# Kernel optimization log

Measured on AMD Instinct MI355X. Metric: run time of the kernel, lower is better.

## Reference

```python
import jax, jax.numpy as jnp
import numpy as np

E = 8            # moe_num_experts
FFN = 8192       # ffn_hidden_size
D = 2048         # d_model
B, T = 1, 4096


def setup_inputs() -> dict:
    key = jax.random.key(0)
    k1, k2, k3, k4 = jax.random.split(key, 4)
    x = jax.random.normal(k1, (B, T, D), dtype=jnp.float32)
    # params stored flat as (E*FFN, D), as in the flax module
    w1 = jax.random.normal(k2, (E * FFN, D), dtype=jnp.float32) * 0.02
    v1 = jax.random.normal(k3, (E * FFN, D), dtype=jnp.float32) * 0.02
    w2 = jax.random.normal(k4, (E * FFN, D), dtype=jnp.float32) * 0.02
    return {"x": x, "w1": w1, "v1": v1, "w2": w2, "expert_idx": 3}


def reference(x, w1, v1, w2, expert_idx):
    # select this expert's weight slabs: (FFN, D) each
    expert_shape = (E, FFN, D)
    ew1 = w1.reshape(expert_shape)[expert_idx]
    ev1 = v1.reshape(expert_shape)[expert_idx]
    ew2 = w2.reshape(expert_shape)[expert_idx]
    # gate and up projections: [B,T,D] x [D,FFN] -> [B,T,FFN]
    x1 = jnp.einsum('btd,fd->btf', x, ew1)
    x2 = jnp.einsum('btd,fd->btf', x, ev1)
    h = jax.nn.silu(x1) * x2
    # down projection (note: matmul with ew2, i.e. contraction over FFN)
    out = jnp.einsum('btf,fd->btd', h, ew2)
    return out
```

## Files before the change

kernel.cpp:

```cpp
#include <hip/hip_runtime.h>

#define E_NUM 8
#define FFN_DIM 8192
#define D_DIM 2048
#define T_DIM 4096

using bf16x8 = __attribute__((ext_vector_type(8))) short;
using f32x4  = __attribute__((ext_vector_type(4))) float;
using u16x8  = __attribute__((ext_vector_type(8))) unsigned short;

__device__ __forceinline__ unsigned short f2bf(float f) {
  union { float f; unsigned int u; } v; v.f = f;
  unsigned int u = v.u;
  unsigned int r = (u + 0x7FFFu + ((u >> 16) & 1u)) >> 16;
  return (unsigned short)r;
}

__device__ __forceinline__ void gload16(const unsigned short* g, const unsigned short* l) {
  __builtin_amdgcn_global_load_lds(
      (const __attribute__((address_space(1))) void*)g,
      (__attribute__((address_space(3))) void*)l, 16, 0, 0);
}

__global__ void convert_kernel(const float* __restrict__ src_base,
                               const int* __restrict__ eidx, long slab,
                               unsigned short* __restrict__ dst, long n) {
  const float* src = src_base + (long)(*eidx) * slab;
  long stride = (long)gridDim.x * blockDim.x;
  for (long i = (long)blockIdx.x * blockDim.x + threadIdx.x; i * 8 < n; i += stride) {
    long e = i * 8;
    const float4* p = (const float4*)(src + e);
    float4 f0 = p[0], f1 = p[1];
    u16x8 o;
    o[0] = f2bf(f0.x); o[1] = f2bf(f0.y); o[2] = f2bf(f0.z); o[3] = f2bf(f0.w);
    o[4] = f2bf(f1.x); o[5] = f2bf(f1.y); o[6] = f2bf(f1.z); o[7] = f2bf(f1.w);
    *(u16x8*)(dst + e) = o;
  }
}

__global__ void transpose_kernel(const float* __restrict__ w2,
                                 const int* __restrict__ eidx,
                                 unsigned short* __restrict__ dst) {
  __shared__ unsigned short tile[32][33];
  const float* src = w2 + (long)(*eidx) * (long)FFN_DIM * D_DIM;
  int d0 = blockIdx.x << 5;
  int f0 = blockIdx.y << 5;
  int tx = threadIdx.x & 31, ty = threadIdx.x >> 5;
#pragma unroll
  for (int i = 0; i < 4; ++i) {
    int f = ty + i * 8;
    tile[f][tx] = f2bf(src[(long)(f0 + f) * D_DIM + d0 + tx]);
  }
  __syncthreads();
#pragma unroll
  for (int i = 0; i < 4; ++i) {
    int d = ty + i * 8;
    dst[(long)(d0 + d) * FFN_DIM + f0 + tx] = tile[tx][d];
  }
}

#define VMCNT8 asm volatile("s_waitcnt vmcnt(8)" ::: "memory")
#define VMCNT6 asm volatile("s_waitcnt vmcnt(6)" ::: "memory")
#define VMCNT2 asm volatile("s_waitcnt vmcnt(2)" ::: "memory")
#define VMCNT0 asm volatile("s_waitcnt vmcnt(0)" ::: "memory")
#define BAR __builtin_amdgcn_s_barrier()

__global__ __launch_bounds__(512, 2) void gemm1_silu(
    const unsigned short* __restrict__ Xb,
    const unsigned short* __restrict__ W1b,
    const unsigned short* __restrict__ V1b,
    unsigned short* __restrict__ Hb) {
  __shared__ __align__(16) unsigned short sA[2 * 256 * 64];
  __shared__ __align__(16) unsigned short sB1[2 * 128 * 64];
  __shared__ __align__(16) unsigned short sB2[2 * 128 * 64];

  const int tid = threadIdx.x;
  const int wv = tid >> 6, l = tid & 63;
  const int wm = wv >> 1, wn = wv & 1;
  const int kq = l >> 4, lr = l & 15;
  const int m0 = blockIdx.y << 8;
  const int n0 = blockIdx.x << 7;

  const int rsub = tid >> 3;
  const int sslot8 = ((tid & 7) ^ ((tid >> 3) & 7)) << 3;
  const unsigned short* gA0  = Xb  + (long)(m0 + rsub) * D_DIM + sslot8;
  const unsigned short* gB1r = W1b + (long)(n0 + rsub) * D_DIM + sslot8;
  const unsigned short* gB2r = V1b + (long)(n0 + rsub) * D_DIM + sslot8;

#define ST_A(r_)  gload16(gA0  + (long)((r_) * 64) * D_DIM + tc, sA  + sb * 16384 + (r_) * 4096 + wv * 512)
#define ST_B1(r_) gload16(gB1r + (long)((r_) * 64) * D_DIM + tc, sB1 + sb * 8192  + (r_) * 4096 + wv * 512)
#define ST_B2(r_) gload16(gB2r + (long)((r_) * 64) * D_DIM + tc, sB2 + sb * 8192  + (r_) * 4096 + wv * 512)

  int raoff[4], rboff[4];
#pragma unroll
  for (int m = 0; m < 4; ++m) {
    int row = wm * 64 + m * 16 + lr;
    raoff[m] = row * 64 + ((kq ^ (row & 7)) << 3);
  }
#pragma unroll
  for (int n = 0; n < 4; ++n) {
    int row = wn * 64 + n * 16 + lr;
    rboff[n] = row * 64 + ((kq ^ (row & 7)) << 3);
  }

  f32x4 acc1[4][4], acc2[4][4];
  f32x4 z = {0.f, 0.f, 0.f, 0.f};
#pragma unroll
  for (int m = 0; m < 4; ++m)
#pragma unroll
    for (int n = 0; n < 4; ++n) { acc1[m][n] = z; acc2[m][n] = z; }

  {
    int tc = 0, sb = 0;
    ST_A(0); ST_A(1); ST_A(2); ST_A(3);
    ST_B1(0); ST_B1(1); ST_B2(0); ST_B2(1);
    VMCNT2;
    BAR;
  }

  const int NT = D_DIM / 64;
  for (int t = 0; t < NT; ++t) {
    const int db = t & 1;
    const unsigned short* Ab  = sA  + db * 16384;
    const unsigned short* B1b = sB1 + db * 8192;
    const unsigned short* B2b = sB2 + db * 8192;
    const int pf = (t < NT - 1);
    const int tc = (t + 1) << 6;
    const int sb = db ^ 1;
    bf16x8 af[4], bf_[4];

#pragma unroll
    for (int m = 0; m < 4; ++m) af[m] = *(const bf16x8*)(Ab + raoff[m]);
#pragma unroll
    for (int n = 0; n < 4; ++n) bf_[n] = *(const bf16x8*)(B1b + rboff[n]);
    if (pf) {
      ST_A(0); ST_A(1); ST_A(2); ST_A(3);
      ST_B1(0); ST_B1(1); ST_B2(0); ST_B2(1);
    }
    BAR;
    __builtin_amdgcn_s_setprio(1);
#pragma unroll
    for (int m = 0; m < 4; ++m)
#pragma unroll
      for (int n = 0; n < 4; ++n)
        acc1[m][n] = __builtin_amdgcn_mfma_f32_16x16x32_bf16(af[m], bf_[n], acc1[m][n], 0, 0, 0);
    __builtin_amdgcn_s_setprio(0);
    if (pf) { VMCNT8; } else { VMCNT0; }
    BAR;

#pragma unroll
    for (int n = 0; n < 4; ++n) bf_[n] = *(const bf16x8*)(B2b + rboff[n]);
    BAR;
    __builtin_amdgcn_s_setprio(1);
#pragma unroll
    for (int m = 0; m < 4; ++m)
#pragma unroll
      for (int n = 0; n < 4; ++n)
        acc2[m][n] = __builtin_amdgcn_mfma_f32_16x16x32_bf16(af[m], bf_[n], acc2[m][n], 0, 0, 0);
    __builtin_amdgcn_s_setprio(0);
    BAR;

#pragma unroll
    for (int m = 0; m < 4; ++m) af[m] = *(const bf16x8*)(Ab + (raoff[m] ^ 32));
#pragma unroll
    for (int n = 0; n < 4; ++n) bf_[n] = *(const bf16x8*)(B1b + (rboff[n] ^ 32));
    BAR;
    __builtin_amdgcn_s_setprio(1);
#pragma unroll
    for (int m = 0; m < 4; ++m)
#pragma unroll
      for (int n = 0; n < 4; ++n)
        acc1[m][n] = __builtin_amdgcn_mfma_f32_16x16x32_bf16(af[m], bf_[n], acc1[m][n], 0, 0, 0);
    __builtin_amdgcn_s_setprio(0);
    BAR;

#pragma unroll
    for (int n = 0; n < 4; ++n) bf_[n] = *(const bf16x8*)(B2b + (rboff[n] ^ 32));
    BAR;
    __builtin_amdgcn_s_setprio(1);
#pragma unroll
    for (int m = 0; m < 4; ++m)
#pragma unroll
      for (int n = 0; n < 4; ++n)
        acc2[m][n] = __builtin_amdgcn_mfma_f32_16x16x32_bf16(af[m], bf_[n], acc2[m][n], 0, 0, 0);
    __builtin_amdgcn_s_setprio(0);
    if (pf) { VMCNT2; }
    BAR;
  }

#pragma unroll
  for (int m = 0; m < 4; ++m)
#pragma unroll
    for (int n = 0; n < 4; ++n)
#pragma unroll
      for (int r = 0; r < 4; ++r) {
        int row = m0 + wm * 64 + m * 16 + kq * 4 + r;
        int col = n0 + wn * 64 + n * 16 + lr;
        float x1 = acc1[m][n][r], x2 = acc2[m][n][r];
        float hv = x1 / (1.f + __expf(-x1)) * x2;
        Hb[(long)row * FFN_DIM + col] = f2bf(hv);
      }
#undef ST_A
#undef ST_B1
#undef ST_B2
}

__global__ __launch_bounds__(512, 2) void gemm2(
    const unsigned short* __restrict__ Hb,
    const unsigned short* __restrict__ W2T,
    float* __restrict__ out) {
  __shared__ __align__(16) unsigned short sA[3 * 256 * 64];
  __shared__ __align__(16) unsigned short sB[3 * 128 * 64];

  const int tid = threadIdx.x;
  const int wv = tid >> 6, l = tid & 63;
  const int wm = wv >> 1, wn = wv & 1;
  const int kq = l >> 4, lr = l & 15;
  const int m0 = blockIdx.y << 8;
  const int n0 = blockIdx.x << 7;

  const int rsub = tid >> 3;
  const int sslot8 = ((tid & 7) ^ ((tid >> 3) & 7)) << 3;
  const unsigned short* gA0  = Hb  + (long)(m0 + rsub) * FFN_DIM + sslot8;
  const unsigned short* gB0r = W2T + (long)(n0 + rsub) * FFN_DIM + sslot8;

#define ST2_A(r_) gload16(gA0  + (long)((r_) * 64) * FFN_DIM + tc2, sA + bwr * 16384 + (r_) * 4096 + wv * 512)
#define ST2_B(r_) gload16(gB0r + (long)((r_) * 64) * FFN_DIM + tc2, sB + bwr * 8192  + (r_) * 4096 + wv * 512)

  int raoff[4], rboff[4];
#pragma unroll
  for (int m = 0; m < 4; ++m) {
    int row = wm * 64 + m * 16 + lr;
    raoff[m] = row * 64 + ((kq ^ (row & 7)) << 3);
  }
#pragma unroll
  for (int n = 0; n < 4; ++n) {
    int row = wn * 64 + n * 16 + lr;
    rboff[n] = row * 64 + ((kq ^ (row & 7)) << 3);
  }

  f32x4 acc[4][4];
  f32x4 z = {0.f, 0.f, 0.f, 0.f};
#pragma unroll
  for (int m = 0; m < 4; ++m)
#pragma unroll
    for (int n = 0; n < 4; ++n) acc[m][n] = z;

  {
    int tc2 = 0, bwr = 0;
    ST2_A(0); ST2_A(1); ST2_A(2); ST2_A(3); ST2_B(0); ST2_B(1);
    tc2 = 64; bwr = 1;
    ST2_A(0); ST2_A(1); ST2_A(2); ST2_A(3); ST2_B(0); ST2_B(1);
    VMCNT6;
    BAR;
  }

  const int NT = FFN_DIM / 64;
  int brd = 0;
  for (int t = 0; t < NT; ++t) {
    const unsigned short* Ab = sA + brd * 16384;
    const unsigned short* Bb = sB + brd * 8192;
    const int pf2 = (t + 2 < NT);
    const int tc2 = (t + 2) << 6;
    const int bwr = (brd + 2 >= 3) ? brd - 1 : brd + 2;
    bf16x8 af[4], bf_[4];

#pragma unroll
    for (int m = 0; m < 4; ++m) af[m] = *(const bf16x8*)(Ab + raoff[m]);
#pragma unroll
    for (int n = 0; n < 4; ++n) bf_[n] = *(const bf16x8*)(Bb + rboff[n]);
    if (pf2) {
      ST2_A(0); ST2_A(1); ST2_A(2); ST2_A(3); ST2_B(0); ST2_B(1);
    }
    BAR;
    __builtin_amdgcn_s_setprio(1);
#pragma unroll
    for (int m = 0; m < 4; ++m)
#pragma unroll
      for (int n = 0; n < 4; ++n)
        acc[m][n] = __builtin_amdgcn_mfma_f32_16x16x32_bf16(af[m], bf_[n], acc[m][n], 0, 0, 0);
    __builtin_amdgcn_s_setprio(0);
    BAR;

#pragma unroll
    for (int m = 0; m < 4; ++m) af[m] = *(const bf16x8*)(Ab + (raoff[m] ^ 32));
#pragma unroll
    for (int n = 0; n < 4; ++n) bf_[n] = *(const bf16x8*)(Bb + (rboff[n] ^ 32));
    BAR;
    __builtin_amdgcn_s_setprio(1);
#pragma unroll
    for (int m = 0; m < 4; ++m)
#pragma unroll
      for (int n = 0; n < 4; ++n)
        acc[m][n] = __builtin_amdgcn_mfma_f32_16x16x32_bf16(af[m], bf_[n], acc[m][n], 0, 0, 0);
    __builtin_amdgcn_s_setprio(0);
    if (pf2) { VMCNT6; } else if (t + 1 < NT) { VMCNT0; }
    BAR;

    brd = (brd + 1 == 3) ? 0 : brd + 1;
  }

#pragma unroll
  for (int m = 0; m < 4; ++m)
#pragma unroll
    for (int n = 0; n < 4; ++n)
#pragma unroll
      for (int r = 0; r < 4; ++r) {
        int row = m0 + wm * 64 + m * 16 + kq * 4 + r;
        int col = n0 + wn * 64 + n * 16 + lr;
        out[(long)row * D_DIM + col] = acc[m][n][r];
      }
#undef ST2_A
#undef ST2_B
}

extern "C" void kernel_launch(void* const* d_in, const int* in_sizes, int n_in,
                              void* d_out, int out_size, void* d_ws, size_t ws_size,
                              hipStream_t stream) {
  const float* x  = (const float*)d_in[0];
  const float* w1 = (const float*)d_in[1];
  const float* v1 = (const float*)d_in[2];
  const float* w2 = (const float*)d_in[3];
  const int* eidx = (const int*)d_in[4];

  char* ws = (char*)d_ws;
  unsigned short* Xb  = (unsigned short*)(ws);
  unsigned short* W1b = (unsigned short*)(ws + (16l << 20));
  unsigned short* V1b = (unsigned short*)(ws + (48l << 20));
  unsigned short* W2T = (unsigned short*)(ws + (80l << 20));
  unsigned short* Hb  = (unsigned short*)(ws + (112l << 20));
  float* out = (float*)d_out;

  long slab = (long)FFN_DIM * D_DIM;
  convert_kernel<<<2048, 256, 0, stream>>>(x,  eidx, 0,    Xb,  (long)T_DIM * D_DIM);
  convert_kernel<<<2048, 256, 0, stream>>>(w1, eidx, slab, W1b, slab);
  convert_kernel<<<2048, 256, 0, stream>>>(v1, eidx, slab, V1b, slab);
  transpose_kernel<<<dim3(D_DIM / 32, FFN_DIM / 32), 256, 0, stream>>>(w2, eidx, W2T);
  gemm1_silu<<<dim3(FFN_DIM / 128, T_DIM / 256), 512, 0, stream>>>(Xb, W1b, V1b, Hb);
  gemm2<<<dim3(D_DIM / 128, T_DIM / 256), 512, 0, stream>>>(Hb, W2T, out);
}
```

Baseline: 538.4 us.

## Restructure both GEMMs into 8-wave ping-pong schedules with staggered per-quadrant prefetch

Both GEMM kernels get a new main loop. It works in four quadrant phases, and each phase issues a slice of the next tiles' global-to-LDS loads, so memory traffic is spread across the iteration instead of bunched in one burst. gemm1 changes its wave layout to 2x4 with each wave covering two 128-row halves, and gemm2 drops from triple to double buffering while splitting A into halves. The goal is better overlap of loads with MFMA work and less LDS use. The trade-offs are more barriers per iteration and tighter vmcnt accounting, where a miscount could expose load latency or give wrong results.

```diff
diff --git a/kernel.cpp b/kernel.cpp
--- a/kernel.cpp
+++ b/kernel.cpp
@@ -59,20 +59,175 @@
   }
 }
 
-#define VMCNT8 asm volatile("s_waitcnt vmcnt(8)" ::: "memory")
 #define VMCNT6 asm volatile("s_waitcnt vmcnt(6)" ::: "memory")
-#define VMCNT2 asm volatile("s_waitcnt vmcnt(2)" ::: "memory")
+#define VMCNT4 asm volatile("s_waitcnt vmcnt(4)" ::: "memory")
 #define VMCNT0 asm volatile("s_waitcnt vmcnt(0)" ::: "memory")
 #define BAR __builtin_amdgcn_s_barrier()
+#define PRIO1 __builtin_amdgcn_s_setprio(1)
+#define PRIO0 __builtin_amdgcn_s_setprio(0)
 
 __global__ __launch_bounds__(512, 2) void gemm1_silu(
     const unsigned short* __restrict__ Xb,
     const unsigned short* __restrict__ W1b,
     const unsigned short* __restrict__ V1b,
     unsigned short* __restrict__ Hb) {
-  __shared__ __align__(16) unsigned short sA[2 * 256 * 64];
-  __shared__ __align__(16) unsigned short sB1[2 * 128 * 64];
-  __shared__ __align__(16) unsigned short sB2[2 * 128 * 64];
+  __shared__ __align__(16) unsigned short sA[2 * 2 * 8192];
+  __shared__ __align__(16) unsigned short sB1[2 * 8192];
+  __shared__ __align__(16) unsigned short sB2[2 * 8192];
+
+  const int tid = threadIdx.x;
+  const int wv = tid >> 6, l = tid & 63;
+  const int wm = wv >> 2, wn = wv & 3;
+  const int kq = l >> 4, lr = l & 15;
+  const int m0 = blockIdx.y << 8;
+  const int n0 = blockIdx.x << 7;
+
+  const int rsub = tid >> 3;
+  const int sslot8 = ((tid & 7) ^ ((tid >> 3) & 7)) << 3;
+  const unsigned short* gA  = Xb  + (long)(m0 + rsub) * D_DIM + sslot8;
+  const unsigned short* gB1 = W1b + (long)(n0 + rsub) * D_DIM + sslot8;
+  const unsigned short* gB2 = V1b + (long)(n0 + rsub) * D_DIM + sslot8;
+
+#define STG(gbase, rowoff, tc_, lbase) do { \
+    gload16((gbase) + (long)(rowoff) * D_DIM + (tc_), (lbase) + wv * 512); \
+    gload16((gbase) + (long)((rowoff) + 64) * D_DIM + (tc_), (lbase) + 4096 + wv * 512); \
+  } while (0)
+
+  int aoff[4], boff[2];
+#pragma unroll
+  for (int j = 0; j < 4; ++j) {
+    int row = wm * 64 + j * 16 + lr;
+    aoff[j] = row * 64 + ((kq ^ (row & 7)) << 3);
+  }
+#pragma unroll
+  for (int g = 0; g < 2; ++g) {
+    int row = wn * 32 + g * 16 + lr;
+    boff[g] = row * 64 + ((kq ^ (row & 7)) << 3);
+  }
+
+  f32x4 acc1[8][2], acc2[8][2];
+  f32x4 z = {0.f, 0.f, 0.f, 0.f};
+#pragma unroll
+  for (int f = 0; f < 8; ++f)
+#pragma unroll
+    for (int g = 0; g < 2; ++g) { acc1[f][g] = z; acc2[f][g] = z; }
+
+  STG(gA, 0, 0, sA);
+  STG(gA, 128, 0, sA + 8192);
+  STG(gB1, 0, 0, sB1);
+  STG(gB2, 0, 0, sB2);
+  STG(gA, 0, 64, sA + 16384);
+  STG(gA, 128, 64, sA + 24576);
+  STG(gB1, 0, 64, sB1 + 8192);
+  VMCNT6;
+  BAR;
+
+  const int NT = D_DIM / 64;
+  for (int t = 0; t < NT; ++t) {
+    const int db = t & 1, sx = db ^ 1;
+    const unsigned short* A0p = sA + (db * 2 + 0) * 8192;
+    const unsigned short* A1p = sA + (db * 2 + 1) * 8192;
+    const unsigned short* B1p = sB1 + db * 8192;
+    const unsigned short* B2p = sB2 + db * 8192;
+    const int p1ok = (t + 1 < NT), p2ok = (t + 2 < NT);
+    const int tc1 = (t + 1) << 6, tc2 = (t + 2) << 6;
+    bf16x8 aA[4][2], aB[4][2], b1[2][2], b2[2][2];
+
+#pragma unroll
+    for (int j = 0; j < 4; ++j) {
+      aA[j][0] = *(const bf16x8*)(A0p + aoff[j]);
+      aA[j][1] = *(const bf16x8*)(A0p + (aoff[j] ^ 32));
+    }
+#pragma unroll
+    for (int g = 0; g < 2; ++g) {
+      b1[g][0] = *(const bf16x8*)(B1p + boff[g]);
+      b1[g][1] = *(const bf16x8*)(B1p + (boff[g] ^ 32));
+    }
+    if (p1ok) STG(gB2, 0, tc1, sB2 + sx * 8192);
+    BAR;
+    PRIO1;
+#pragma unroll
+    for (int j = 0; j < 4; ++j)
+#pragma unroll
+      for (int g = 0; g < 2; ++g) {
+        acc1[j][g] = __builtin_amdgcn_mfma_f32_16x16x32_bf16(aA[j][0], b1[g][0], acc1[j][g], 0, 0, 0);
+        acc1[j][g] = __builtin_amdgcn_mfma_f32_16x16x32_bf16(aA[j][1], b1[g][1], acc1[j][g], 0, 0, 0);
+      }
+    PRIO0;
+    BAR;
+
+#pragma unroll
+    for (int j = 0; j < 4; ++j) {
+      aB[j][0] = *(const bf16x8*)(A1p + aoff[j]);
+      aB[j][1] = *(const bf16x8*)(A1p + (aoff[j] ^ 32));
+    }
+    if (p2ok) STG(gA, 0, tc2, sA + (db * 2 + 0) * 8192);
+    BAR;
+    PRIO1;
+#pragma unroll
+    for (int j = 0; j < 4; ++j)
+#pragma unroll
+      for (int g = 0; g < 2; ++g) {
+        acc1[4 + j][g] = __builtin_amdgcn_mfma_f32_16x16x32_bf16(aB[j][0], b1[g][0], acc1[4 + j][g], 0, 0, 0);
+        acc1[4 + j][g] = __builtin_amdgcn_mfma_f32_16x16x32_bf16(aB[j][1], b1[g][1], acc1[4 + j][g], 0, 0, 0);
+      }
+    PRIO0;
+    BAR;
+
+#pragma unroll
+    for (int g = 0; g < 2; ++g) {
+      b2[g][0] = *(const bf16x8*)(B2p + boff[g]);
+      b2[g][1] = *(const bf16x8*)(B2p + (boff[g] ^ 32));
+    }
+    if (p2ok) STG(gA, 128, tc2, sA + (db * 2 + 1) * 8192);
+    BAR;
+    PRIO1;
+#pragma unroll
+    for (int j = 0; j < 4; ++j)
+#pragma unroll
+      for (int g = 0; g < 2; ++g) {
+        acc2[j][g] = __builtin_amdgcn_mfma_f32_16x16x32_bf16(aA[j][0], b2[g][0], acc2[j][g], 0, 0, 0);
+        acc2[j][g] = __builtin_amdgcn_mfma_f32_16x16x32_bf16(aA[j][1], b2[g][1], acc2[j][g], 0, 0, 0);
+      }
+    PRIO0;
+    BAR;
+
+    if (p2ok) STG(gB1, 0, tc2, sB1 + db * 8192);
+    BAR;
+    PRIO1;
+#pragma unroll
+    for (int j = 0; j < 4; ++j)
+#pragma unroll
+      for (int g = 0; g < 2; ++g) {
+        acc2[4 + j][g] = __builtin_amdgcn_mfma_f32_16x16x32_bf16(aB[j][0], b2[g][0], acc2[4 + j][g], 0, 0, 0);
+        acc2[4 + j][g] = __builtin_amdgcn_mfma_f32_16x16x32_bf16(aB[j][1], b2[g][1], acc2[4 + j][g], 0, 0, 0);
+      }
+    PRIO0;
+    if (p2ok) { VMCNT6; } else if (p1ok) { VMCNT0; }
+    BAR;
+  }
+
+#pragma unroll
+  for (int f = 0; f < 8; ++f)
+#pragma unroll
+    for (int g = 0; g < 2; ++g)
+#pragma unroll
+      for (int r = 0; r < 4; ++r) {
+        int row = m0 + (f >> 2) * 128 + wm * 64 + (f & 3) * 16 + kq * 4 + r;
+        int col = n0 + wn * 32 + g * 16 + lr;
+        float x1 = acc1[f][g][r], x2 = acc2[f][g][r];
+        float hv = x1 / (1.f + __expf(-x1)) * x2;
+        Hb[(long)row * FFN_DIM + col] = f2bf(hv);
+      }
+#undef STG
+}
+
+__global__ __launch_bounds__(512, 2) void gemm2(
+    const unsigned short* __restrict__ Hb,
+    const unsigned short* __restrict__ W2T,
+    float* __restrict__ out) {
+  __shared__ __align__(16) unsigned short sA[2 * 2 * 8192];
+  __shared__ __align__(16) unsigned short sB[2 * 8192];
 
   const int tid = threadIdx.x;
   const int wv = tid >> 6, l = tid & 63;
@@ -80,238 +235,138 @@
   const int kq = l >> 4, lr = l & 15;
   const int m0 = blockIdx.y << 8;
   const int n0 = blockIdx.x << 7;
+  const int hA = wm >> 1;
 
   const int rsub = tid >> 3;
   const int sslot8 = ((tid & 7) ^ ((tid >> 3) & 7)) << 3;
-  const unsigned short* gA0  = Xb  + (long)(m0 + rsub) * D_DIM + sslot8;
-  const unsigned short* gB1r = W1b + (long)(n0 + rsub) * D_DIM + sslot8;
-  const unsigned short* gB2r = V1b + (long)(n0 + rsub) * D_DIM + sslot8;
-
-#define ST_A(r_)  gload16(gA0  + (long)((r_) * 64) * D_DIM + tc, sA  + sb * 16384 + (r_) * 4096 + wv * 512)
-#define ST_B1(r_) gload16(gB1r + (long)((r_) * 64) * D_DIM + tc, sB1 + sb * 8192  + (r_) * 4096 + wv * 512)
-#define ST_B2(r_) gload16(gB2r + (long)((r_) * 64) * D_DIM + tc, sB2 + sb * 8192  + (r_) * 4096 + wv * 512)
-
-  int raoff[4], rboff[4];
-#pragma unroll
-  for (int m = 0; m < 4; ++m) {
-    int row = wm * 64 + m * 16 + lr;
-    raoff[m] = row * 64 + ((kq ^ (row & 7)) << 3);
-  }
-#pragma unroll
-  for (int n = 0; n < 4; ++n) {
-    int row = wn * 64 + n * 16 + lr;
-    rboff[n] = row * 64 + ((kq ^ (row & 7)) << 3);
-  }
-
-  f32x4 acc1[4][4], acc2[4][4];
-  f32x4 z = {0.f, 0.f, 0.f, 0.f};
-#pragma unroll
-  for (int m = 0; m < 4; ++m)
-#pragma unroll
-    for (int n = 0; n < 4; ++n) { acc1[m][n] = z; acc2[m][n] = z; }
-
-  {
-    int tc = 0, sb = 0;
-    ST_A(0); ST_A(1); ST_A(2); ST_A(3);
-    ST_B1(0); ST_B1(1); ST_B2(0); ST_B2(1);
-    VMCNT2;
-    BAR;
-  }
-
-  const int NT = D_DIM / 64;
-  for (int t = 0; t < NT; ++t) {
-    const int db = t & 1;
-    const unsigned short* Ab  = sA  + db * 16384;
-    const unsigned short* B1b = sB1 + db * 8192;
-    const unsigned short* B2b = sB2 + db * 8192;
-    const int pf = (t < NT - 1);
-    const int tc = (t + 1) << 6;
-    const int sb = db ^ 1;
-    bf16x8 af[4], bf_[4];
-
-#pragma unroll
-    for (int m = 0; m < 4; ++m) af[m] = *(const bf16x8*)(Ab + raoff[m]);
-#pragma unroll
-    for (int n = 0; n < 4; ++n) bf_[n] = *(const bf16x8*)(B1b + rboff[n]);
-    if (pf) {
-      ST_A(0); ST_A(1); ST_A(2); ST_A(3);
-      ST_B1(0); ST_B1(1); ST_B2(0); ST_B2(1);
-    }
-    BAR;
-    __builtin_amdgcn_s_setprio(1);
-#pragma unroll
-    for (int m = 0; m < 4; ++m)
-#pragma unroll
-      for (int n = 0; n < 4; ++n)
-        acc1[m][n] = __builtin_amdgcn_mfma_f32_16x16x32_bf16(af[m], bf_[n], acc1[m][n], 0, 0, 0);
-    __builtin_amdgcn_s_setprio(0);
-    if (pf) { VMCNT8; } else { VMCNT0; }
-    BAR;
-
-#pragma unroll
-    for (int n = 0; n < 4; ++n) bf_[n] = *(const bf16x8*)(B2b + rboff[n]);
-    BAR;
-    __builtin_amdgcn_s_setprio(1);
-#pragma unroll
-    for (int m = 0; m < 4; ++m)
-#pragma unroll
-      for (int n = 0; n < 4; ++n)
-        acc2[m][n] = __builtin_amdgcn_mfma_f32_16x16x32_bf16(af[m], bf_[n], acc2[m][n], 0, 0, 0);
-    __builtin_amdgcn_s_setprio(0);
-    BAR;
-
-#pragma unroll
-    for (int m = 0; m < 4; ++m) af[m] = *(const bf16x8*)(Ab + (raoff[m] ^ 32));
-#pragma unroll
-    for (int n = 0; n < 4; ++n) bf_[n] = *(const bf16x8*)(B1b + (rboff[n] ^ 32));
-    BAR;
-    __builtin_amdgcn_s_setprio(1);
-#pragma unroll
-    for (int m = 0; m < 4; ++m)
-#pragma unroll
-      for (int n = 0; n < 4; ++n)
-        acc1[m][n] = __builtin_amdgcn_mfma_f32_16x16x32_bf16(af[m], bf_[n], acc1[m][n], 0, 0, 0);
-    __builtin_amdgcn_s_setprio(0);
-    BAR;
-
-#pragma unroll
-    for (int n = 0; n < 4; ++n) bf_[n] = *(const bf16x8*)(B2b + (rboff[n] ^ 32));
-    BAR;
-    __builtin_amdgcn_s_setprio(1);
-#pragma unroll
-    for (int m = 0; m < 4; ++m)
-#pragma unroll
-      for (int n = 0; n < 4; ++n)
-        acc2[m][n] = __builtin_amdgcn_mfma_f32_16x16x32_bf16(af[m], bf_[n], acc2[m][n], 0, 0, 0);
-    __builtin_amdgcn_s_setprio(0);
-    if (pf) { VMCNT2; }
-    BAR;
-  }
-
-#pragma unroll
-  for (int m = 0; m < 4; ++m)
-#pragma unroll
-    for (int n = 0; n < 4; ++n)
-#pragma unroll
-      for (int r = 0; r < 4; ++r) {
-        int row = m0 + wm * 64 + m * 16 + kq * 4 + r;
-        int col = n0 + wn * 64 + n * 16 + lr;
-        float x1 = acc1[m][n][r], x2 = acc2[m][n][r];
-        float hv = x1 / (1.f + __expf(-x1)) * x2;
-        Hb[(long)row * FFN_DIM + col] = f2bf(hv);
-      }
-#undef ST_A
-#undef ST_B1
-#undef ST_B2
-}
-
-__global__ __launch_bounds__(512, 2) void gemm2(
-    const unsigned short* __restrict__ Hb,
-    const unsigned short* __restrict__ W2T,
-    float* __restrict__ out) {
-  __shared__ __align__(16) unsigned short sA[3 * 256 * 64];
-  __shared__ __align__(16) unsigned short sB[3 * 128 * 64];
-
-  const int tid = threadIdx.x;
-  const int wv = tid >> 6, l = tid & 63;
-  const int wm = wv >> 1, wn = wv & 1;
-  const int kq = l >> 4, lr = l & 15;
-  const int m0 = blockIdx.y << 8;
-  const int n0 = blockIdx.x << 7;
-
-  const int rsub = tid >> 3;
-  const int sslot8 = ((tid & 7) ^ ((tid >> 3) & 7)) << 3;
-  const unsigned short* gA0  = Hb  + (long)(m0 + rsub) * FFN_DIM + sslot8;
-  const unsigned short* gB0r = W2T + (long)(n0 + rsub) * FFN_DIM + sslot8;
-
-#define ST2_A(r_) gload16(gA0  + (long)((r_) * 64) * FFN_DIM + tc2, sA + bwr * 16384 + (r_) * 4096 + wv * 512)
-#define ST2_B(r_) gload16(gB0r + (long)((r_) * 64) * FFN_DIM + tc2, sB + bwr * 8192  + (r_) * 4096 + wv * 512)
-
-  int raoff[4], rboff[4];
-#pragma unroll
-  for (int m = 0; m < 4; ++m) {
-    int row = wm * 64 + m * 16 + lr;
-    raoff[m] = row * 64 + ((kq ^ (row & 7)) << 3);
-  }
-#pragma unroll
-  for (int n = 0; n < 4; ++n) {
-    int row = wn * 64 + n * 16 + lr;
-    rboff[n] = row * 64 + ((kq ^ (row & 7)) << 3);
+  const unsigned short* gA = Hb  + (long)(m0 + rsub) * FFN_DIM + sslot8;
+  const unsigned short* gB = W2T + (long)(n0 + rsub) * FFN_DIM + sslot8;
+
+#define STG2(gbase, rowoff, tc_, lbase) do { \
+    gload16((gbase) + (long)(rowoff) * FFN_DIM + (tc_), (lbase) + wv * 512); \
+    gload16((gbase) + (long)((rowoff) + 64) * FFN_DIM + (tc_), (lbase) + 4096 + wv * 512); \
+  } while (0)
+
+  int aoff[4], boff[4];
+#pragma unroll
+  for (int f = 0; f < 4; ++f) {
+    int row = (wm & 1) * 64 + f * 16 + lr;
+    aoff[f] = row * 64 + ((kq ^ (row & 7)) << 3);
+  }
+#pragma unroll
+  for (int g = 0; g < 4; ++g) {
+    int row = wn * 64 + g * 16 + lr;
+    boff[g] = row * 64 + ((kq ^ (row & 7)) << 3);
   }
 
   f32x4 acc[4][4];
   f32x4 z = {0.f, 0.f, 0.f, 0.f};
 #pragma unroll
-  for (int m = 0; m < 4; ++m)
-#pragma unroll
-    for (int n = 0; n < 4; ++n) acc[m][n] = z;
-
-  {
-    int tc2 = 0, bwr = 0;
-    ST2_A(0); ST2_A(1); ST2_A(2); ST2_A(3); ST2_B(0); ST2_B(1);
-    tc2 = 64; bwr = 1;
-    ST2_A(0); ST2_A(1); ST2_A(2); ST2_A(3); ST2_B(0); ST2_B(1);
-    VMCNT6;
-    BAR;
-  }
+  for (int f = 0; f < 4; ++f)
+#pragma unroll
+    for (int g = 0; g < 4; ++g) acc[f][g] = z;
+
+  STG2(gA, 0, 0, sA);
+  STG2(gA, 128, 0, sA + 8192);
+  STG2(gB, 0, 0, sB);
+  STG2(gA, 0, 64, sA + 16384);
+  STG2(gA, 128, 64, sA + 24576);
+  VMCNT4;
+  BAR;
 
   const int NT = FFN_DIM / 64;
-  int brd = 0;
   for (int t = 0; t < NT; ++t) {
-    const unsigned short* Ab = sA + brd * 16384;
-    const unsigned short* Bb = sB + brd * 8192;
-    const int pf2 = (t + 2 < NT);
-    const int tc2 = (t + 2) << 6;
-    const int bwr = (brd + 2 >= 3) ? brd - 1 : brd + 2;
-    bf16x8 af[4], bf_[4];
-
-#pragma unroll
-    for (int m = 0; m < 4; ++m) af[m] = *(const bf16x8*)(Ab + raoff[m]);
-#pragma unroll
-    for (int n = 0; n < 4; ++n) bf_[n] = *(const bf16x8*)(Bb + rboff[n]);
-    if (pf2) {
-      ST2_A(0); ST2_A(1); ST2_A(2); ST2_A(3); ST2_B(0); ST2_B(1);
-    }
-    BAR;
-    __builtin_amdgcn_s_setprio(1);
-#pragma unroll
-    for (int m = 0; m < 4; ++m)
-#pragma unroll
-      for (int n = 0; n < 4; ++n)
-        acc[m][n] = __builtin_amdgcn_mfma_f32_16x16x32_bf16(af[m], bf_[n], acc[m][n], 0, 0, 0);
-    __builtin_amdgcn_s_setprio(0);
-    BAR;
-
-#pragma unroll
-    for (int m = 0; m < 4; ++m) af[m] = *(const bf16x8*)(Ab + (raoff[m] ^ 32));
-#pragma unroll
-    for (int n = 0; n < 4; ++n) bf_[n] = *(const bf16x8*)(Bb + (rboff[n] ^ 32));
-    BAR;
-    __builtin_amdgcn_s_setprio(1);
-#pragma unroll
-    for (int m = 0; m < 4; ++m)
-#pragma unroll
-      for (int n = 0; n < 4; ++n)
-        acc[m][n] = __builtin_amdgcn_mfma_f32_16x16x32_bf16(af[m], bf_[n], acc[m][n], 0, 0, 0);
-    __builtin_amdgcn_s_setprio(0);
-    if (pf2) { VMCNT6; } else if (t + 1 < NT) { VMCNT0; }
-    BAR;
-
-    brd = (brd + 1 == 3) ? 0 : brd + 1;
-  }
-
-#pragma unroll
-  for (int m = 0; m < 4; ++m)
-#pragma unroll
-    for (int n = 0; n < 4; ++n)
+    const int db = t & 1, sx = db ^ 1;
+    const unsigned short* Ap = sA + (db * 2 + hA) * 8192;
+    const unsigned short* Bp = sB + db * 8192;
+    const int p1ok = (t + 1 < NT), p2ok = (t + 2 < NT);
+    const int tc1 = (t + 1) << 6, tc2 = (t + 2) << 6;
+    bf16x8 aA[2][2], aB[2][2], bA[2][2], bB[2][2];
+
+#pragma unroll
+    for (int f = 0; f < 2; ++f) {
+      aA[f][0] = *(const bf16x8*)(Ap + aoff[f]);
+      aA[f][1] = *(const bf16x8*)(Ap + (aoff[f] ^ 32));
+    }
+#pragma unroll
+    for (int g = 0; g < 2; ++g) {
+      bA[g][0] = *(const bf16x8*)(Bp + boff[g]);
+      bA[g][1] = *(const bf16x8*)(Bp + (boff[g] ^ 32));
+    }
+    if (p1ok) STG2(gB, 0, tc1, sB + sx * 8192);
+    BAR;
+    PRIO1;
+#pragma unroll
+    for (int f = 0; f < 2; ++f)
+#pragma unroll
+      for (int g = 0; g < 2; ++g) {
+        acc[f][g] = __builtin_amdgcn_mfma_f32_16x16x32_bf16(aA[f][0], bA[g][0], acc[f][g], 0, 0, 0);
+        acc[f][g] = __builtin_amdgcn_mfma_f32_16x16x32_bf16(aA[f][1], bA[g][1], acc[f][g], 0, 0, 0);
+      }
+    PRIO0;
+    BAR;
+
+#pragma unroll
+    for (int f = 0; f < 2; ++f) {
+      aB[f][0] = *(const bf16x8*)(Ap + aoff[2 + f]);
+      aB[f][1] = *(const bf16x8*)(Ap + (aoff[2 + f] ^ 32));
+    }
+    BAR;
+    PRIO1;
+#pragma unroll
+    for (int f = 0; f < 2; ++f)
+#pragma unroll
+      for (int g = 0; g < 2; ++g) {
+        acc[2 + f][g] = __builtin_amdgcn_mfma_f32_16x16x32_bf16(aB[f][0], bA[g][0], acc[2 + f][g], 0, 0, 0);
+        acc[2 + f][g] = __builtin_amdgcn_mfma_f32_16x16x32_bf16(aB[f][1], bA[g][1], acc[2 + f][g], 0, 0, 0);
+      }
+    PRIO0;
+    BAR;
+
+#pragma unroll
+    for (int g = 0; g < 2; ++g) {
+      bB[g][0] = *(const bf16x8*)(Bp + boff[2 + g]);
+      bB[g][1] = *(const bf16x8*)(Bp + (boff[2 + g] ^ 32));
+    }
+    if (p2ok) STG2(gA, 0, tc2, sA + (db * 2 + 0) * 8192);
+    BAR;
+    PRIO1;
+#pragma unroll
+    for (int f = 0; f < 2; ++f)
+#pragma unroll
+      for (int g = 0; g < 2; ++g) {
+        acc[f][2 + g] = __builtin_amdgcn_mfma_f32_16x16x32_bf16(aA[f][0], bB[g][0], acc[f][2 + g], 0, 0, 0);
+        acc[f][2 + g] = __builtin_amdgcn_mfma_f32_16x16x32_bf16(aA[f][1], bB[g][1], acc[f][2 + g], 0, 0, 0);
+      }
+    PRIO0;
+    BAR;
+
+    if (p2ok) STG2(gA, 128, tc2, sA + (db * 2 + 1) * 8192);
+    BAR;
+    PRIO1;
+#pragma unroll
+    for (int f = 0; f < 2; ++f)
+#pragma unroll
+      for (int g = 0; g < 2; ++g) {
+        acc[2 + f][2 + g] = __builtin_amdgcn_mfma_f32_16x16x32_bf16(aB[f][0], bB[g][0], acc[2 + f][2 + g], 0, 0, 0);
+        acc[2 + f][2 + g] = __builtin_amdgcn_mfma_f32_16x16x32_bf16(aB[f][1], bB[g][1], acc[2 + f][2 + g], 0, 0, 0);
+      }
+    PRIO0;
+    if (p2ok) { VMCNT4; } else if (p1ok) { VMCNT0; }
+    BAR;
+  }
+
+#pragma unroll
+  for (int f = 0; f < 4; ++f)
+#pragma unroll
+    for (int g = 0; g < 4; ++g)
 #pragma unroll
       for (int r = 0; r < 4; ++r) {
-        int row = m0 + wm * 64 + m * 16 + kq * 4 + r;
-        int col = n0 + wn * 64 + n * 16 + lr;
-        out[(long)row * D_DIM + col] = acc[m][n][r];
-      }
-#undef ST2_A
-#undef ST2_B
+        int row = m0 + wm * 64 + f * 16 + kq * 4 + r;
+        int col = n0 + wn * 64 + g * 16 + lr;
+        out[(long)row * D_DIM + col] = acc[f][g][r];
+      }
+#undef STG2
 }
 
 extern "C" void kernel_launch(void* const* d_in, const int* in_sizes, int n_in,
```

Result: faster. 491.6 us (-8.7%).
